# Optimization experiments

Hardware: AMD Instinct MI355X
Metric: run time of the kernel (lower is better)

## Reference

```python
import jax, jax.numpy as jnp
import numpy as np

B, T, D, H, E = 4, 2048, 1024, 1024, 8
NEG_SLOPE = 0.01  # torch LeakyReLU default

def leaky_relu(x):
    return jnp.where(x >= 0, x, NEG_SLOPE * x)

def setup_inputs() -> dict:
    key = jax.random.key(0)
    ks = jax.random.split(key, 10)
    s = 0.02
    return {
        "x": jax.random.normal(ks[0], (B, T, D), jnp.float32),
        "gate_w": jax.random.normal(ks[1], (D, E), jnp.float32) * s,
        "gate_b": jnp.zeros((E,), jnp.float32),
        "w1": jax.random.normal(ks[2], (E, D, H), jnp.float32) * s,
        "b1": jnp.zeros((E, H), jnp.float32),
        "w2": jax.random.normal(ks[3], (E, H, H), jnp.float32) * s,
        "b2": jnp.zeros((E, H), jnp.float32),
        "w3": jax.random.normal(ks[4], (E, H, D), jnp.float32) * s,
        "b3": jnp.zeros((E, D), jnp.float32),
        "topn": 2,
    }

def reference(x, gate_w, gate_b, w1, b1, w2, b2, w3, b3, topn):
    # Gating: softmax over experts, top-k mask, L1 renormalize
    gating = jax.nn.softmax(x @ gate_w + gate_b, axis=-1)          # [B,T,E]
    _, topk_idx = jax.lax.top_k(gating, topn)                       # [B,T,k]
    mask = jax.nn.one_hot(topk_idx, E, dtype=gating.dtype).sum(-2)  # [B,T,E]
    g = gating * mask
    g = g / jnp.maximum(jnp.sum(jnp.abs(g), axis=-1, keepdims=True), 1e-12)
    # Dense all-expert MLP: Linear -> LeakyReLU -> Linear -> LeakyReLU -> Linear
    h = leaky_relu(jnp.einsum('btd,edh->bteh', x, w1) + b1)         # [B,T,E,H]
    h = leaky_relu(jnp.einsum('bteh,ehg->bteg', h, w2) + b2)        # [B,T,E,H]
    eo = jnp.einsum('bteh,ehd->bted', h, w3) + b3                   # [B,T,E,D]
    # Weighted combine
    return jnp.einsum('bte,bted->btd', g, eo)                       # [B,T,D]
```

## Files before the change

### kernel.cpp

```cpp
#include <hip/hip_runtime.h>
#include <hip/hip_bf16.h>
#include <stdint.h>

#define TOKENS   8192
#define DDIM     1024
#define EXPERTS  8
#define NSLOT    (TOKENS * 2)
#define MAXTILE  136

typedef __bf16 bf16x8_t __attribute__((ext_vector_type(8)));
typedef __bf16 bf16x4_t __attribute__((ext_vector_type(4)));
typedef float  f32x4_t  __attribute__((ext_vector_type(4)));

__device__ __forceinline__ void gl_lds16(const void* g, void* l) {
  __builtin_amdgcn_global_load_lds(
      (const __attribute__((address_space(1))) void*)g,
      (__attribute__((address_space(3))) void*)l, 16, 0, 0);
}

__global__ void twt_k(const float* __restrict__ w1, const float* __restrict__ w2,
                      const float* __restrict__ w3, __bf16* __restrict__ w1T,
                      __bf16* __restrict__ w2T, __bf16* __restrict__ w3T) {
  __shared__ float tile[64][33];
  const int layer = blockIdx.z >> 3, e = blockIdx.z & 7;
  const float* w = (layer == 0) ? w1 : (layer == 1) ? w2 : w3;
  __bf16* wT = (layer == 0) ? w1T : (layer == 1) ? w2T : w3T;
  const int kb = blockIdx.x * 64, nb = blockIdx.y * 32;
  const size_t ebase = (size_t)e << 20;
  const int tx = threadIdx.x, ty = threadIdx.y;
  const float* src = w + ebase;
#pragma unroll
  for (int r = ty; r < 64; r += 8)
    tile[r][tx] = src[(size_t)(kb + r) * 1024 + nb + tx];
  __syncthreads();
  __bf16* dst = wT + ebase;
#pragma unroll
  for (int r = ty; r < 32; r += 8) {
    union { __bf16 h[2]; unsigned u; } pk;
    pk.h[0] = (__bf16)tile[2 * tx][r];
    pk.h[1] = (__bf16)tile[2 * tx + 1][r];
    *(unsigned*)(dst + (size_t)(nb + r) * 1024 + kb + 2 * tx) = pk.u;
  }
}

__global__ __launch_bounds__(256) void gate_k(
    const float* __restrict__ x, const float* __restrict__ gw,
    const float* __restrict__ gb, __bf16* __restrict__ xbf,
    int* __restrict__ top_i, float* __restrict__ top_w) {
  const int t = blockIdx.x * 4 + (threadIdx.x >> 6);
  const int lane = threadIdx.x & 63;
  const float4* x4 = (const float4*)(x + (size_t)t * DDIM);
  bf16x4_t* xo4 = (bf16x4_t*)(xbf + (size_t)t * DDIM);
  const float4* g4 = (const float4*)gw;
  float acc[EXPERTS];
#pragma unroll
  for (int e = 0; e < EXPERTS; ++e) acc[e] = 0.f;
#pragma unroll
  for (int d4 = lane; d4 < 256; d4 += 64) {
    const float4 v = x4[d4];
    bf16x4_t o = {(__bf16)v.x, (__bf16)v.y, (__bf16)v.z, (__bf16)v.w};
    xo4[d4] = o;
    const float4* g = g4 + (size_t)d4 * 8;
    float4 ga, gbv;
    ga = g[0]; gbv = g[1];
    acc[0] += v.x * ga.x; acc[1] += v.x * ga.y; acc[2] += v.x * ga.z; acc[3] += v.x * ga.w;
    acc[4] += v.x * gbv.x; acc[5] += v.x * gbv.y; acc[6] += v.x * gbv.z; acc[7] += v.x * gbv.w;
    ga = g[2]; gbv = g[3];
    acc[0] += v.y * ga.x; acc[1] += v.y * ga.y; acc[2] += v.y * ga.z; acc[3] += v.y * ga.w;
    acc[4] += v.y * gbv.x; acc[5] += v.y * gbv.y; acc[6] += v.y * gbv.z; acc[7] += v.y * gbv.w;
    ga = g[4]; gbv = g[5];
    acc[0] += v.z * ga.x; acc[1] += v.z * ga.y; acc[2] += v.z * ga.z; acc[3] += v.z * ga.w;
    acc[4] += v.z * gbv.x; acc[5] += v.z * gbv.y; acc[6] += v.z * gbv.z; acc[7] += v.z * gbv.w;
    ga = g[6]; gbv = g[7];
    acc[0] += v.w * ga.x; acc[1] += v.w * ga.y; acc[2] += v.w * ga.z; acc[3] += v.w * ga.w;
    acc[4] += v.w * gbv.x; acc[5] += v.w * gbv.y; acc[6] += v.w * gbv.z; acc[7] += v.w * gbv.w;
  }
#pragma unroll
  for (int e = 0; e < EXPERTS; ++e)
    for (int s = 32; s > 0; s >>= 1) acc[e] += __shfl_down(acc[e], s);
  if (lane == 0) {
#pragma unroll
    for (int e = 0; e < EXPERTS; ++e) acc[e] += gb[e];
    int i1 = 0;
    for (int e = 1; e < EXPERTS; ++e)
      if (acc[e] > acc[i1]) i1 = e;
    int i2 = (i1 == 0) ? 1 : 0;
    for (int e = 0; e < EXPERTS; ++e)
      if (e != i1 && acc[e] > acc[i2]) i2 = e;
    const float r = expf(acc[i2] - acc[i1]);
    const float wA = 1.f / (1.f + r);
    const float wB = r / (1.f + r);
    top_i[t * 2] = i1; top_i[t * 2 + 1] = i2;
    top_w[t * 2] = wA; top_w[t * 2 + 1] = wB;
  }
}

__global__ __launch_bounds__(1024) void plan_k(
    const int* __restrict__ top_i, int* __restrict__ eoff,
    int* __restrict__ tok_list, int* __restrict__ slot_of,
    int* __restrict__ work, int* __restrict__ ntiles) {
  const int tid = threadIdx.x;
  const int lane = tid & 63, wid = tid >> 6;
  __shared__ int ws[16][EXPERTS];
  __shared__ int eoff_s[EXPERTS];
  __shared__ int base_lds[1024 * EXPERTS];

  int ids[16];
  unsigned long long h64 = 0;
#pragma unroll
  for (int j = 0; j < 16; ++j) {
    ids[j] = top_i[tid * 16 + j];
    h64 += 1ull << (ids[j] * 8);
  }
#pragma unroll
  for (int e = 0; e < EXPERTS; ++e) {
    const int h = (int)((h64 >> (8 * e)) & 0xff);
    int v = h;
    for (int s = 1; s < 64; s <<= 1) {
      const int u = __shfl_up(v, s);
      if (lane >= s) v += u;
    }
    const int excl = v - h;
    const int tot = __shfl(v, 63);
    if (lane == 0) ws[wid][e] = tot;
    base_lds[tid * EXPERTS + e] = excl;
  }
  __syncthreads();
  if (tid == 0) {
    int tot[EXPERTS];
    for (int e = 0; e < EXPERTS; ++e) {
      int run = 0;
      for (int w = 0; w < 16; ++w) { const int c = ws[w][e]; ws[w][e] = run; run += c; }
      tot[e] = run;
    }
    int s = 0, nt = 0;
    for (int e = 0; e < EXPERTS; ++e) {
      eoff_s[e] = s; eoff[e] = s; s += tot[e];
      const int mt = (tot[e] + 127) >> 7;
      for (int i = 0; i < mt; ++i) work[nt++] = (e << 16) | i;
    }
    eoff[EXPERTS] = s;
    ntiles[0] = nt;
  }
  __syncthreads();
#pragma unroll
  for (int e = 0; e < EXPERTS; ++e)
    base_lds[tid * EXPERTS + e] += eoff_s[e] + ws[wid][e];
  unsigned long long pre64 = 0;
#pragma unroll
  for (int j = 0; j < 16; ++j) {
    const int entry = tid * 16 + j;
    const int e = ids[j];
    const int pre = (int)((pre64 >> (8 * e)) & 0xff);
    pre64 += 1ull << (8 * e);
    const int s = base_lds[tid * EXPERTS + e] + pre;
    tok_list[s] = entry >> 1;
    slot_of[entry] = s;
  }
}

template <int GATHER, int LEAKY>
__global__ __launch_bounds__(256) void moe_gemm(
    const __bf16* __restrict__ A, const int* __restrict__ tok,
    const __bf16* __restrict__ W, const float* __restrict__ bias,
    const int* __restrict__ eoff, const int* __restrict__ work,
    const int* __restrict__ ntiles, __bf16* __restrict__ out) {
  if ((int)blockIdx.y >= ntiles[0]) return;
  const int wk = work[blockIdx.y];
  const int e = wk >> 16;
  const int m0 = (wk & 0xffff) * 128;
  const int off = eoff[e];
  const int ne = eoff[e + 1] - off;
  const int n0 = blockIdx.x * 128;

  __shared__ __align__(16) __bf16 As[128 * 32];
  __shared__ __align__(16) __bf16 Bs[128 * 32];

  const int tid = threadIdx.x;
  const int lane = tid & 63;
  const int wid = tid >> 6;
  const int wm = wid >> 1, wn = wid & 1;
  const int ln = lane & 15, quad = lane >> 4;

  const __bf16* aptr[2];
  const __bf16* bptr[2];
  __bf16* alds[2];
  __bf16* blds[2];
#pragma unroll
  for (int j = 0; j < 2; ++j) {
    const int c = (wid * 2 + j) * 64 + lane;
    const int row = c >> 2;
    const int kc = (c & 3) ^ ((row >> 1) & 3);
    int r = m0 + row;
    if (r >= ne) r = m0;
    const long arow = GATHER ? (long)tok[off + r] : (long)(off + r);
    aptr[j] = A + arow * DDIM + kc * 8;
    alds[j] = (__bf16*)As + (wid * 2 + j) * 512;
    bptr[j] = W + ((long)e << 20) + (long)(n0 + row) * 1024 + kc * 8;
    blds[j] = (__bf16*)Bs + (wid * 2 + j) * 512;
  }

  const int swz = (quad ^ ((ln >> 1) & 3)) * 8;

  const f32x4_t vzero = {0.f, 0.f, 0.f, 0.f};
  f32x4_t acc[4][4];
#pragma unroll
  for (int i = 0; i < 4; ++i)
#pragma unroll
    for (int j = 0; j < 4; ++j) acc[i][j] = vzero;

  for (int kt = 0; kt < 32; ++kt) {
    const int k0 = kt * 32;
    __syncthreads();
    gl_lds16(aptr[0] + k0, alds[0]);
    gl_lds16(aptr[1] + k0, alds[1]);
    gl_lds16(bptr[0] + k0, blds[0]);
    gl_lds16(bptr[1] + k0, blds[1]);
    __syncthreads();

    bf16x8_t aF[4], bF[4];
#pragma unroll
    for (int i = 0; i < 4; ++i)
      aF[i] = *(const bf16x8_t*)(As + (wm * 64 + i * 16 + ln) * 32 + swz);
#pragma unroll
    for (int j = 0; j < 4; ++j)
      bF[j] = *(const bf16x8_t*)(Bs + (wn * 64 + j * 16 + ln) * 32 + swz);
#pragma unroll
    for (int i = 0; i < 4; ++i)
#pragma unroll
      for (int j = 0; j < 4; ++j)
        acc[i][j] = __builtin_amdgcn_mfma_f32_16x16x32_bf16(aF[i], bF[j],
                                                            acc[i][j], 0, 0, 0);
  }

  const float* bs = bias + e * 1024;
#pragma unroll
  for (int i = 0; i < 4; ++i) {
    const int rloc = wm * 64 + i * 16 + quad * 4;
#pragma unroll
    for (int j = 0; j < 4; ++j) {
      const int col = n0 + wn * 64 + j * 16 + ln;
      const float bv = bs[col];
#pragma unroll
      for (int r = 0; r < 4; ++r) {
        const int m = m0 + rloc + r;
        if (m < ne) {
          float v = acc[i][j][r] + bv;
          if (LEAKY) v = (v >= 0.f) ? v : 0.01f * v;
          out[(size_t)(off + m) * 1024 + col] = (__bf16)v;
        }
      }
    }
  }
}

__global__ __launch_bounds__(256) void combine_k(
    const __bf16* __restrict__ eo, const int* __restrict__ slot_of,
    const float* __restrict__ top_w, float* __restrict__ out) {
  const int t = blockIdx.x;
  const int s1 = slot_of[t * 2], s2 = slot_of[t * 2 + 1];
  const float w1 = top_w[t * 2], w2 = top_w[t * 2 + 1];
  const bf16x4_t a = ((const bf16x4_t*)(eo + (size_t)s1 * DDIM))[threadIdx.x];
  const bf16x4_t b = ((const bf16x4_t*)(eo + (size_t)s2 * DDIM))[threadIdx.x];
  float4 o;
  o.x = w1 * (float)a[0] + w2 * (float)b[0];
  o.y = w1 * (float)a[1] + w2 * (float)b[1];
  o.z = w1 * (float)a[2] + w2 * (float)b[2];
  o.w = w1 * (float)a[3] + w2 * (float)b[3];
  ((float4*)(out + (size_t)t * DDIM))[threadIdx.x] = o;
}

extern "C" void kernel_launch(void* const* d_in, const int* in_sizes, int n_in,
                              void* d_out, int out_size, void* d_ws,
                              size_t ws_size, hipStream_t stream) {
  (void)in_sizes; (void)n_in; (void)out_size; (void)ws_size;
  const float* x  = (const float*)d_in[0];
  const float* gw = (const float*)d_in[1];
  const float* gb = (const float*)d_in[2];
  const float* w1 = (const float*)d_in[3];
  const float* b1 = (const float*)d_in[4];
  const float* w2 = (const float*)d_in[5];
  const float* b2 = (const float*)d_in[6];
  const float* w3 = (const float*)d_in[7];
  const float* b3 = (const float*)d_in[8];
  float* out = (float*)d_out;

  uint8_t* p = (uint8_t*)d_ws;
  auto alloc = [&](size_t b) {
    uint8_t* r = p;
    p += (b + 255) & ~(size_t)255;
    return r;
  };
  int*    eoff     = (int*)alloc(4 * (EXPERTS + 1));
  int*    ntiles   = (int*)alloc(4);
  int*    work     = (int*)alloc(4 * MAXTILE);
  int*    top_i    = (int*)alloc(4ull * TOKENS * 2);
  float*  top_w    = (float*)alloc(4ull * TOKENS * 2);
  int*    slot_of  = (int*)alloc(4ull * TOKENS * 2);
  int*    tok_list = (int*)alloc(4ull * NSLOT);
  __bf16* xbf      = (__bf16*)alloc(2ull * TOKENS * DDIM);
  __bf16* w1T      = (__bf16*)alloc(2ull * EXPERTS * 1024 * 1024);
  __bf16* w2T      = (__bf16*)alloc(2ull * EXPERTS * 1024 * 1024);
  __bf16* w3T      = (__bf16*)alloc(2ull * EXPERTS * 1024 * 1024);
  __bf16* h1       = (__bf16*)alloc(2ull * NSLOT * 1024);
  __bf16* h2       = (__bf16*)alloc(2ull * NSLOT * 1024);
  __bf16* eo       = (__bf16*)alloc(2ull * NSLOT * 1024);

  gate_k<<<TOKENS / 4, 256, 0, stream>>>(x, gw, gb, xbf, top_i, top_w);
  twt_k<<<dim3(16, 32, 24), dim3(32, 8), 0, stream>>>(w1, w2, w3, w1T, w2T, w3T);
  plan_k<<<1, 1024, 0, stream>>>(top_i, eoff, tok_list, slot_of, work, ntiles);

  moe_gemm<1, 1><<<dim3(8, MAXTILE), 256, 0, stream>>>(
      xbf, tok_list, w1T, b1, eoff, work, ntiles, h1);
  moe_gemm<0, 1><<<dim3(8, MAXTILE), 256, 0, stream>>>(
      h1, tok_list, w2T, b2, eoff, work, ntiles, h2);
  moe_gemm<0, 0><<<dim3(8, MAXTILE), 256, 0, stream>>>(
      h2, tok_list, w3T, b3, eoff, work, ntiles, eo);

  combine_k<<<TOKENS, 256, 0, stream>>>(eo, slot_of, top_w, out);
}
```

Before: 437.7 us.

## Load MFMA operands directly from global memory with register double-buffering, drop LDS

Replaces the LDS-staged GEMM main loop (global_load_lds into shared tiles with two barriers per k-step) with direct per-lane global vector loads into MFMA fragment registers, double-buffered across k-steps. This removes the shared memory and all __syncthreads from the inner loop. The cost is that each wave now fetches its own A and B fragments, so the tiles shared between the two waves of each row or column are read twice from global/L2, and the 16-byte per-lane loads stride across rows. The tok_list allocation is padded.

Result: slower. 719.1 us (+64.3%).

```diff
diff --git a/kernel.cpp b/kernel.cpp
--- a/kernel.cpp
+++ b/kernel.cpp
@@ -11,12 +11,6 @@
 typedef __bf16 bf16x8_t __attribute__((ext_vector_type(8)));
 typedef __bf16 bf16x4_t __attribute__((ext_vector_type(4)));
 typedef float  f32x4_t  __attribute__((ext_vector_type(4)));
-
-__device__ __forceinline__ void gl_lds16(const void* g, void* l) {
-  __builtin_amdgcn_global_load_lds(
-      (const __attribute__((address_space(1))) void*)g,
-      (__attribute__((address_space(3))) void*)l, 16, 0, 0);
-}
 
 __global__ void twt_k(const float* __restrict__ w1, const float* __restrict__ w2,
                       const float* __restrict__ w3, __bf16* __restrict__ w1T,
@@ -173,34 +167,24 @@
   const int ne = eoff[e + 1] - off;
   const int n0 = blockIdx.x * 128;
 
-  __shared__ __align__(16) __bf16 As[128 * 32];
-  __shared__ __align__(16) __bf16 Bs[128 * 32];
-
-  const int tid = threadIdx.x;
-  const int lane = tid & 63;
-  const int wid = tid >> 6;
+  const int lane = threadIdx.x & 63;
+  const int wid = threadIdx.x >> 6;
   const int wm = wid >> 1, wn = wid & 1;
   const int ln = lane & 15, quad = lane >> 4;
 
-  const __bf16* aptr[2];
-  const __bf16* bptr[2];
-  __bf16* alds[2];
-  __bf16* blds[2];
-#pragma unroll
-  for (int j = 0; j < 2; ++j) {
-    const int c = (wid * 2 + j) * 64 + lane;
-    const int row = c >> 2;
-    const int kc = (c & 3) ^ ((row >> 1) & 3);
-    int r = m0 + row;
-    if (r >= ne) r = m0;
-    const long arow = GATHER ? (long)tok[off + r] : (long)(off + r);
-    aptr[j] = A + arow * DDIM + kc * 8;
-    alds[j] = (__bf16*)As + (wid * 2 + j) * 512;
-    bptr[j] = W + ((long)e << 20) + (long)(n0 + row) * 1024 + kc * 8;
-    blds[j] = (__bf16*)Bs + (wid * 2 + j) * 512;
-  }
-
-  const int swz = (quad ^ ((ln >> 1) & 3)) * 8;
+  const __bf16* arow[4];
+#pragma unroll
+  for (int i = 0; i < 4; ++i) {
+    int m = m0 + wm * 64 + i * 16 + ln;
+    if (m >= ne) m = 0;
+    const long r = GATHER ? (long)tok[off + m] : (long)(off + m);
+    arow[i] = A + r * DDIM + quad * 8;
+  }
+  const __bf16* brow[4];
+#pragma unroll
+  for (int j = 0; j < 4; ++j)
+    brow[j] = W + ((long)e << 20) +
+              (long)(n0 + wn * 64 + j * 16 + ln) * 1024 + quad * 8;
 
   const f32x4_t vzero = {0.f, 0.f, 0.f, 0.f};
   f32x4_t acc[4][4];
@@ -209,27 +193,36 @@
 #pragma unroll
     for (int j = 0; j < 4; ++j) acc[i][j] = vzero;
 
-  for (int kt = 0; kt < 32; ++kt) {
-    const int k0 = kt * 32;
-    __syncthreads();
-    gl_lds16(aptr[0] + k0, alds[0]);
-    gl_lds16(aptr[1] + k0, alds[1]);
-    gl_lds16(bptr[0] + k0, blds[0]);
-    gl_lds16(bptr[1] + k0, blds[1]);
-    __syncthreads();
-
-    bf16x8_t aF[4], bF[4];
+  bf16x8_t aP[4], bP[4], aQ[4], bQ[4];
+#pragma unroll
+  for (int i = 0; i < 4; ++i) {
+    aP[i] = *(const bf16x8_t*)(arow[i]);
+    bP[i] = *(const bf16x8_t*)(brow[i]);
+  }
+  for (int kt = 0; kt < 32; kt += 2) {
+    const int kQ = (kt + 1) * 32;
+#pragma unroll
+    for (int i = 0; i < 4; ++i) {
+      aQ[i] = *(const bf16x8_t*)(arow[i] + kQ);
+      bQ[i] = *(const bf16x8_t*)(brow[i] + kQ);
+    }
 #pragma unroll
     for (int i = 0; i < 4; ++i)
-      aF[i] = *(const bf16x8_t*)(As + (wm * 64 + i * 16 + ln) * 32 + swz);
-#pragma unroll
-    for (int j = 0; j < 4; ++j)
-      bF[j] = *(const bf16x8_t*)(Bs + (wn * 64 + j * 16 + ln) * 32 + swz);
+#pragma unroll
+      for (int j = 0; j < 4; ++j)
+        acc[i][j] = __builtin_amdgcn_mfma_f32_16x16x32_bf16(aP[i], bP[j],
+                                                            acc[i][j], 0, 0, 0);
+    const int kP = (kt + 2 < 32) ? (kt + 2) * 32 : 0;
+#pragma unroll
+    for (int i = 0; i < 4; ++i) {
+      aP[i] = *(const bf16x8_t*)(arow[i] + kP);
+      bP[i] = *(const bf16x8_t*)(brow[i] + kP);
+    }
 #pragma unroll
     for (int i = 0; i < 4; ++i)
 #pragma unroll
       for (int j = 0; j < 4; ++j)
-        acc[i][j] = __builtin_amdgcn_mfma_f32_16x16x32_bf16(aF[i], bF[j],
+        acc[i][j] = __builtin_amdgcn_mfma_f32_16x16x32_bf16(aQ[i], bQ[j],
                                                             acc[i][j], 0, 0, 0);
   }
 
@@ -297,7 +290,7 @@
   int*    top_i    = (int*)alloc(4ull * TOKENS * 2);
   float*  top_w    = (float*)alloc(4ull * TOKENS * 2);
   int*    slot_of  = (int*)alloc(4ull * TOKENS * 2);
-  int*    tok_list = (int*)alloc(4ull * NSLOT);
+  int*    tok_list = (int*)alloc(4ull * (NSLOT + 256));
   __bf16* xbf      = (__bf16*)alloc(2ull * TOKENS * DDIM);
   __bf16* w1T      = (__bf16*)alloc(2ull * EXPERTS * 1024 * 1024);
   __bf16* w2T      = (__bf16*)alloc(2ull * EXPERTS * 1024 * 1024);
```
